# Kernel optimization log

Hardware: AMD Instinct MI355X
Metric: run time of the kernel (lower is better)

Reference implementation:

```python
import jax, jax.numpy as jnp
import numpy as np

DIM = 192
HEADS = 6
WIN = (2, 6, 12)          # (pl, lat, lon)
TOW = 64                  # type_of_windows = (8//2)*(96//6)
N_TOK = WIN[0] * WIN[1] * WIN[2]            # 144
TABLE_ROWS = WIN[0]**2 * WIN[1]**2 * (2 * WIN[2] - 1)  # 3312


def calc_position_bias_indices(size):
    pl, la, lo = size
    plq = np.arange(pl); plk = -np.arange(pl) * pl
    laq = np.arange(la); lak = -np.arange(la) * la
    lon = np.arange(lo)
    gq = np.stack(np.meshgrid(plq, laq, lon, indexing='ij'))  # [3,pl,la,lo]
    gk = np.stack(np.meshgrid(plk, lak, lon, indexing='ij'))
    fq = gq.reshape(3, -1)
    fk = gk.reshape(3, -1)
    d = fq[:, :, None] - fk[:, None, :]          # [3,N,N]
    d = np.transpose(d, (1, 2, 0)).copy()
    d[:, :, 2] += lo - 1
    d[:, :, 1] *= 2 * lo - 1
    d[:, :, 0] *= (2 * lo - 1) * la * la
    return d.sum(-1)                              # [N,N]


def setup_inputs() -> dict:
    key = jax.random.key(0)
    ks = jax.random.split(key, 7)
    B_, nW, N, C = 15, TOW, N_TOK, DIM
    x = jax.random.normal(ks[0], (B_, nW, N, C), jnp.float32)
    mask = jax.random.normal(ks[1], (15, nW, N, N), jnp.float32)  # nLon=15
    qkv_w = jax.random.normal(ks[2], (3 * C, C), jnp.float32) * 0.02
    qkv_b = jnp.zeros((3 * C,), jnp.float32)
    table = jax.random.normal(ks[3], (TABLE_ROWS, TOW, HEADS), jnp.float32) * 0.02
    proj_w = jax.random.normal(ks[4], (C, C), jnp.float32) * 0.02
    proj_b = jnp.zeros((C,), jnp.float32)
    pos_index = jnp.asarray(calc_position_bias_indices(WIN), jnp.int32)  # [N,N]
    return {"x": x, "mask": mask, "qkv_w": qkv_w, "qkv_b": qkv_b,
            "table": table, "proj_w": proj_w, "proj_b": proj_b,
            "pos_index": pos_index}


def reference(x, mask, qkv_w, qkv_b, table, proj_w, proj_b, pos_index):
    B_, nW, N, C = x.shape
    h = HEADS
    hd = C // h
    scale = hd ** -0.5
    # qkv projection -> (3, B_, h, nW, N, hd)
    qkv = (jnp.einsum('bwnc,dc->bwnd', x, qkv_w) + qkv_b)
    qkv = qkv.reshape(B_, nW, N, 3, h, hd).transpose(3, 0, 4, 1, 2, 5)
    q, k, v = qkv[0] * scale, qkv[1], qkv[2]
    attn = jnp.einsum('bhwqd,bhwkd->bhwqk', q, k)      # [B_,h,nW,N,N]
    # gather earth position bias: [N,N,tow,h] -> [h,tow,N,N]
    bias = table[pos_index.reshape(-1)].reshape(N, N, nW, h)
    bias = bias.transpose(3, 2, 0, 1)
    attn = attn + bias[None]
    nLon = mask.shape[0]
    attn = attn.reshape(B_ // nLon, nLon, h, nW, N, N) + mask[None, :, None]
    attn = attn.reshape(B_, h, nW, N, N)
    attn = jax.nn.softmax(attn, axis=-1)
    out = jnp.einsum('bhwqk,bhwkd->bhwqd', attn, v)
    out = out.transpose(0, 2, 3, 1, 4).reshape(B_, nW, N, C)
    return jnp.einsum('bwnc,dc->bwnd', out, proj_w) + proj_b
```

## Files before the change

kernel.cpp:

```cpp
#include <hip/hip_runtime.h>

#define HEADS 6
#define N_TOK 144
#define DIM   192
#define NW    64
#define NB    15
#define NBW   (NB * NW)
#define CHUNK 480

typedef __attribute__((ext_vector_type(8))) short bf16x8;
typedef __attribute__((ext_vector_type(4))) float f32x4;

#define MFMA(a, b, c) __builtin_amdgcn_mfma_f32_16x16x32_bf16(a, b, c, 0, 0, 0)

static __device__ __forceinline__ short f2bf(float f) {
    union { float f; unsigned u; } v; v.f = f;
    unsigned r = v.u + 0x7FFFu + ((v.u >> 16) & 1u);
    return (short)(r >> 16);
}
static __device__ __forceinline__ float bf2f(short s) {
    union { unsigned u; float f; } v;
    v.u = ((unsigned)(unsigned short)s) << 16;
    return v.f;
}

__global__ __launch_bounds__(256)
void bias_k(const float* __restrict__ table, const int* __restrict__ pos_index,
            short* __restrict__ bias_bf) {
    const int t = blockIdx.x;
    for (int e = threadIdx.x; e < N_TOK * N_TOK; e += 256) {
        int idx = pos_index[e];
        bias_bf[(long)t * (N_TOK * N_TOK) + e] = f2bf(table[(long)idx * 384 + t]);
    }
}

__global__ __launch_bounds__(256)
void cvt_k(const float* __restrict__ w, short* __restrict__ o, int n) {
    int i = blockIdx.x * 256 + threadIdx.x;
    if (i < n) o[i] = f2bf(w[i]);
}

__global__ __launch_bounds__(256)
void cvtx_k(const float* __restrict__ x, short* __restrict__ xb, int n4) {
    int i = blockIdx.x * 256 + threadIdx.x;
    if (i < n4) {
        float4 f = ((const float4*)x)[i];
        short4 s = { f2bf(f.x), f2bf(f.y), f2bf(f.z), f2bf(f.w) };
        ((short4*)xb)[i] = s;
    }
}

__global__ __launch_bounds__(576)
void qkvs_k(const short* __restrict__ xb, const short* __restrict__ qkvw_bf,
            const float* __restrict__ qkv_b, short* __restrict__ qkv_out) {
    __shared__ short wlds[192 * 200];

    const int sel = blockIdx.x % 3;
    const int bwL = blockIdx.x / 3;
    const int tid = threadIdx.x;

    for (int u = tid * 8; u < 192 * 192; u += 576 * 8) {
        int r = u / 192, c = u - r * 192;
        *(bf16x8*)&wlds[r * 200 + c] = *(const bf16x8*)&qkvw_bf[sel * 36864 + u];
    }
    __syncthreads();

    const int wid = tid >> 6, lane = tid & 63, lq = lane & 15, lg = lane >> 4;
    const int mg = wid / 3, ng = wid % 3;
    const short* xrow = xb + (long)bwL * N_TOK * DIM;

    f32x4 acc[3][4] = {};
    for (int ks = 0; ks < 6; ++ks) {
        const int k0 = ks * 32 + 8 * lg;
        bf16x8 av[3], bv[4];
        #pragma unroll
        for (int mt = 0; mt < 3; ++mt)
            av[mt] = *(const bf16x8*)&xrow[(mg * 48 + mt * 16 + lq) * DIM + k0];
        #pragma unroll
        for (int nt = 0; nt < 4; ++nt)
            bv[nt] = *(const bf16x8*)&wlds[(ng * 64 + nt * 16 + lq) * 200 + k0];
        #pragma unroll
        for (int mt = 0; mt < 3; ++mt)
            #pragma unroll
            for (int nt = 0; nt < 4; ++nt)
                acc[mt][nt] = MFMA(av[mt], bv[nt], acc[mt][nt]);
    }
    __syncthreads();

    const float scale = 0.17677669529663687f;
    #pragma unroll
    for (int nt = 0; nt < 4; ++nt) {
        const int cd = ng * 64 + nt * 16 + lq;
        const float bb = qkv_b[sel * 192 + cd];
        #pragma unroll
        for (int mt = 0; mt < 3; ++mt)
            #pragma unroll
            for (int i = 0; i < 4; ++i) {
                int row = mg * 48 + mt * 16 + 4 * lg + i;
                float v = acc[mt][nt][i] + bb;
                if (sel == 0) v *= scale;
                wlds[row * 200 + cd] = f2bf(v);
            }
    }
    __syncthreads();

    short* ob = qkv_out + (long)bwL * 6 * 3 * 4608 + (long)sel * 4608;
    #pragma unroll
    for (int j = 0; j < 6; ++j) {
        int u = (j * 576 + tid) * 8;
        int h = u / 4608, rem = u - h * 4608;
        int row = rem >> 5, e = rem & 31;
        *(bf16x8*)&ob[(long)h * 3 * 4608 + rem] =
            *(const bf16x8*)&wlds[row * 200 + h * 32 + e];
    }
}

__global__ __launch_bounds__(576)
void attnproj_k(const short* __restrict__ qkv, const short* __restrict__ bias_bf,
                const float* __restrict__ mask, const short* __restrict__ pwt,
                const float* __restrict__ proj_b, float* __restrict__ out,
                int bw0) {
    __shared__ short pw_s[9 * 16 * 152];
    __shared__ short vlds[32 * 152];
    __shared__ short outb[N_TOK * 200];

    const int bwL = blockIdx.x;
    const int bwG = bw0 + bwL;
    const int tid = threadIdx.x;
    const int lane = tid & 63, lq = lane & 15, lg = lane >> 4;
    const int wid = tid >> 6;
    const int m0 = wid * 16;
    const int w = bwG & 63;
    const float* mp = mask + (long)bwG * (N_TOK * N_TOK);
    short* pw = pw_s + wid * 16 * 152;

    #pragma unroll 1
    for (int h = 0; h < HEADS; ++h) {
        const short* qb = qkv + ((long)(bwL * 6 + h) * 3) * 4608;
        const short* kb = qb + 4608;
        const short* vb = qb + 9216;

        __syncthreads();
        {
            int j = tid >> 2, e0 = (tid & 3) * 8;
            bf16x8 vv = *(const bf16x8*)&vb[j * 32 + e0];
            #pragma unroll
            for (int u = 0; u < 8; ++u) vlds[(e0 + u) * 152 + j] = vv[u];
        }
        __syncthreads();

        const f32x4 zf = {};
        bf16x8 aq = *(const bf16x8*)&qb[(m0 + lq) * 32 + 8 * lg];
        f32x4 lgt[9];
        #pragma unroll
        for (int nt = 0; nt < 9; ++nt) {
            bf16x8 bk = *(const bf16x8*)&kb[(nt * 16 + lq) * 32 + 8 * lg];
            lgt[nt] = MFMA(aq, bk, zf);
        }

        const short* bp = bias_bf + (long)(w * 6 + h) * (N_TOK * N_TOK);
        #pragma unroll
        for (int nt = 0; nt < 9; ++nt)
            #pragma unroll
            for (int i = 0; i < 4; ++i) {
                int r = m0 + 4 * lg + i, c = nt * 16 + lq;
                lgt[nt][i] += bf2f(bp[r * N_TOK + c]) + mp[r * N_TOK + c];
            }

        float inv_s[4];
        #pragma unroll
        for (int i = 0; i < 4; ++i) {
            float m = lgt[0][i];
            #pragma unroll
            for (int nt = 1; nt < 9; ++nt) m = fmaxf(m, lgt[nt][i]);
            m = fmaxf(m, __shfl_xor(m, 1));
            m = fmaxf(m, __shfl_xor(m, 2));
            m = fmaxf(m, __shfl_xor(m, 4));
            m = fmaxf(m, __shfl_xor(m, 8));
            float s = 0.f;
            #pragma unroll
            for (int nt = 0; nt < 9; ++nt) {
                float p = __expf(lgt[nt][i] - m);
                lgt[nt][i] = p;
                s += p;
            }
            s += __shfl_xor(s, 1);
            s += __shfl_xor(s, 2);
            s += __shfl_xor(s, 4);
            s += __shfl_xor(s, 8);
            inv_s[i] = 1.f / s;
        }

        #pragma unroll
        for (int nt = 0; nt < 9; ++nt)
            #pragma unroll
            for (int i = 0; i < 4; ++i)
                pw[(4 * lg + i) * 152 + nt * 16 + lq] = f2bf(lgt[nt][i]);

        f32x4 o[2] = {};
        const bf16x8 zb = {};
        #pragma unroll
        for (int ks = 0; ks < 5; ++ks) {
            bf16x8 ap = *(const bf16x8*)&pw[lq * 152 + ks * 32 + 8 * lg];
            #pragma unroll
            for (int nt = 0; nt < 2; ++nt) {
                bf16x8 bv = *(const bf16x8*)&vlds[(nt * 16 + lq) * 152 + ks * 32 + 8 * lg];
                if (ks == 4 && lg >= 2) { ap = zb; bv = zb; }
                o[nt] = MFMA(ap, bv, o[nt]);
            }
        }

        #pragma unroll
        for (int nt = 0; nt < 2; ++nt)
            #pragma unroll
            for (int i = 0; i < 4; ++i) {
                int row = m0 + 4 * lg + i;
                outb[row * 200 + h * 32 + nt * 16 + lq] = f2bf(o[nt][i] * inv_s[i]);
            }
    }
    __syncthreads();

    f32x4 acc[12] = {};
    for (int ks = 0; ks < 6; ++ks) {
        const int k0 = ks * 32 + 8 * lg;
        bf16x8 a = *(const bf16x8*)&outb[(m0 + lq) * 200 + k0];
        #pragma unroll
        for (int nt = 0; nt < 12; ++nt) {
            bf16x8 b = *(const bf16x8*)&pwt[(nt * 16 + lq) * DIM + k0];
            acc[nt] = MFMA(a, b, acc[nt]);
        }
    }
    float* ob = out + (long)bwG * N_TOK * DIM;
    #pragma unroll
    for (int nt = 0; nt < 12; ++nt) {
        float pb = proj_b[nt * 16 + lq];
        #pragma unroll
        for (int i = 0; i < 4; ++i)
            ob[(m0 + 4 * lg + i) * DIM + nt * 16 + lq] = acc[nt][i] + pb;
    }
}

extern "C" void kernel_launch(void* const* d_in, const int* in_sizes, int n_in,
                              void* d_out, int out_size, void* d_ws, size_t ws_size,
                              hipStream_t stream) {
    const float* x        = (const float*)d_in[0];
    const float* mask     = (const float*)d_in[1];
    const float* qkv_w    = (const float*)d_in[2];
    const float* qkv_b    = (const float*)d_in[3];
    const float* table    = (const float*)d_in[4];
    const float* proj_w   = (const float*)d_in[5];
    const float* proj_b   = (const float*)d_in[6];
    const int*   pos_index= (const int*)d_in[7];
    float* out = (float*)d_out;

    short* bias_bf  = (short*)d_ws;
    short* projw_bf = bias_bf + (size_t)384 * N_TOK * N_TOK;
    short* qkvw_bf  = projw_bf + 36864;
    short* xbf_ws   = qkvw_bf + 110592;
    short* qkv_ws   = xbf_ws + (size_t)CHUNK * N_TOK * DIM;

    bias_k<<<384, 256, 0, stream>>>(table, pos_index, bias_bf);
    cvt_k<<<144, 256, 0, stream>>>(proj_w, projw_bf, DIM * DIM);
    cvt_k<<<432, 256, 0, stream>>>(qkv_w, qkvw_bf, 3 * DIM * DIM);

    const int n4 = CHUNK * N_TOK * DIM / 4;
    for (int c = 0; c < 2; ++c) {
        const int bw0 = c * CHUNK;
        cvtx_k<<<(n4 + 255) / 256, 256, 0, stream>>>(
            x + (long)bw0 * N_TOK * DIM, xbf_ws, n4);
        qkvs_k<<<CHUNK * 3, 576, 0, stream>>>(xbf_ws, qkvw_bf, qkv_b, qkv_ws);
        attnproj_k<<<CHUNK, 576, 0, stream>>>(qkv_ws, bias_bf, mask, projw_bf,
                                              proj_b, out, bw0);
    }
}
```

Measured before the change: 533.2 us.

## Transpose attention MFMA layout, hoist mask loads, split projection into separate kernel

The attention kernel now computes K·Q^T, so each lane owns one query row. Softmax reductions then need only two cross-lane shuffles, and bias and mask can be read as vector loads, with the mask held in registers across all heads. Probabilities are staged through a small per-wave LDS tile, one k-tile at a time, which shrinks LDS use. The output projection moves to a separate kernel that reads a bf16 temporary buffer reusing the x workspace. This trades a global round trip and an extra launch for higher occupancy in the attention kernel.

```diff
diff --git a/kernel.cpp b/kernel.cpp
--- a/kernel.cpp
+++ b/kernel.cpp
@@ -23,6 +23,10 @@
     v.u = ((unsigned)(unsigned short)s) << 16;
     return v.f;
 }
+static __device__ __forceinline__ unsigned pk2(float a, float b) {
+    return (unsigned)(unsigned short)f2bf(a) |
+           ((unsigned)(unsigned short)f2bf(b) << 16);
+}
 
 __global__ __launch_bounds__(256)
 void bias_k(const float* __restrict__ table, const int* __restrict__ pos_index,
@@ -116,23 +120,28 @@
 }
 
 __global__ __launch_bounds__(576)
-void attnproj_k(const short* __restrict__ qkv, const short* __restrict__ bias_bf,
-                const float* __restrict__ mask, const short* __restrict__ pwt,
-                const float* __restrict__ proj_b, float* __restrict__ out,
-                int bw0) {
-    __shared__ short pw_s[9 * 16 * 152];
+void attn3_k(const short* __restrict__ qkv, const short* __restrict__ bias_bf,
+             const float* __restrict__ mask, short* __restrict__ tmp, int bw0) {
     __shared__ short vlds[32 * 152];
-    __shared__ short outb[N_TOK * 200];
+    __shared__ short pws[9 * 16 * 40];
 
     const int bwL = blockIdx.x;
     const int bwG = bw0 + bwL;
     const int tid = threadIdx.x;
     const int lane = tid & 63, lq = lane & 15, lg = lane >> 4;
     const int wid = tid >> 6;
-    const int m0 = wid * 16;
+    const int q = wid * 16 + lq;
     const int w = bwG & 63;
-    const float* mp = mask + (long)bwG * (N_TOK * N_TOK);
-    short* pw = pw_s + wid * 16 * 152;
+
+    const float* mp = mask + (long)bwG * (N_TOK * N_TOK) + q * N_TOK + 4 * lg;
+    float4 mreg[9];
+    #pragma unroll
+    for (int nt = 0; nt < 9; ++nt) mreg[nt] = *(const float4*)&mp[nt * 16];
+
+    short* pw = pws + wid * 16 * 40;
+    short* tb = tmp + (long)bwL * N_TOK * DIM + q * DIM;
+    const f32x4 zf = {};
+    const bf16x8 zb = {};
 
     #pragma unroll 1
     for (int h = 0; h < HEADS; ++h) {
@@ -149,81 +158,91 @@
         }
         __syncthreads();
 
-        const f32x4 zf = {};
-        bf16x8 aq = *(const bf16x8*)&qb[(m0 + lq) * 32 + 8 * lg];
+        bf16x8 bq = *(const bf16x8*)&qb[q * 32 + 8 * lg];
         f32x4 lgt[9];
         #pragma unroll
         for (int nt = 0; nt < 9; ++nt) {
-            bf16x8 bk = *(const bf16x8*)&kb[(nt * 16 + lq) * 32 + 8 * lg];
-            lgt[nt] = MFMA(aq, bk, zf);
-        }
-
-        const short* bp = bias_bf + (long)(w * 6 + h) * (N_TOK * N_TOK);
+            bf16x8 ak = *(const bf16x8*)&kb[(nt * 16 + lq) * 32 + 8 * lg];
+            lgt[nt] = MFMA(ak, bq, zf);
+        }
+
+        const short* bp = bias_bf + (long)(w * 6 + h) * (N_TOK * N_TOK)
+                        + q * N_TOK + 4 * lg;
+        #pragma unroll
+        for (int nt = 0; nt < 9; ++nt) {
+            short4 bs = *(const short4*)&bp[nt * 16];
+            lgt[nt][0] += bf2f(bs.x) + mreg[nt].x;
+            lgt[nt][1] += bf2f(bs.y) + mreg[nt].y;
+            lgt[nt][2] += bf2f(bs.z) + mreg[nt].z;
+            lgt[nt][3] += bf2f(bs.w) + mreg[nt].w;
+        }
+
+        float m = lgt[0][0];
         #pragma unroll
         for (int nt = 0; nt < 9; ++nt)
             #pragma unroll
+            for (int i = 0; i < 4; ++i) m = fmaxf(m, lgt[nt][i]);
+        m = fmaxf(m, __shfl_xor(m, 16));
+        m = fmaxf(m, __shfl_xor(m, 32));
+        float s = 0.f;
+        #pragma unroll
+        for (int nt = 0; nt < 9; ++nt)
+            #pragma unroll
             for (int i = 0; i < 4; ++i) {
-                int r = m0 + 4 * lg + i, c = nt * 16 + lq;
-                lgt[nt][i] += bf2f(bp[r * N_TOK + c]) + mp[r * N_TOK + c];
-            }
-
-        float inv_s[4];
-        #pragma unroll
-        for (int i = 0; i < 4; ++i) {
-            float m = lgt[0][i];
-            #pragma unroll
-            for (int nt = 1; nt < 9; ++nt) m = fmaxf(m, lgt[nt][i]);
-            m = fmaxf(m, __shfl_xor(m, 1));
-            m = fmaxf(m, __shfl_xor(m, 2));
-            m = fmaxf(m, __shfl_xor(m, 4));
-            m = fmaxf(m, __shfl_xor(m, 8));
-            float s = 0.f;
-            #pragma unroll
-            for (int nt = 0; nt < 9; ++nt) {
                 float p = __expf(lgt[nt][i] - m);
                 lgt[nt][i] = p;
                 s += p;
             }
-            s += __shfl_xor(s, 1);
-            s += __shfl_xor(s, 2);
-            s += __shfl_xor(s, 4);
-            s += __shfl_xor(s, 8);
-            inv_s[i] = 1.f / s;
-        }
-
-        #pragma unroll
-        for (int nt = 0; nt < 9; ++nt)
-            #pragma unroll
-            for (int i = 0; i < 4; ++i)
-                pw[(4 * lg + i) * 152 + nt * 16 + lq] = f2bf(lgt[nt][i]);
+        s += __shfl_xor(s, 16);
+        s += __shfl_xor(s, 32);
+        const float inv = 1.f / s;
 
         f32x4 o[2] = {};
-        const bf16x8 zb = {};
-        #pragma unroll
-        for (int ks = 0; ks < 5; ++ks) {
-            bf16x8 ap = *(const bf16x8*)&pw[lq * 152 + ks * 32 + 8 * lg];
-            #pragma unroll
-            for (int nt = 0; nt < 2; ++nt) {
-                bf16x8 bv = *(const bf16x8*)&vlds[(nt * 16 + lq) * 152 + ks * 32 + 8 * lg];
-                if (ks == 4 && lg >= 2) { ap = zb; bv = zb; }
-                o[nt] = MFMA(ap, bv, o[nt]);
-            }
-        }
-
-        #pragma unroll
-        for (int nt = 0; nt < 2; ++nt)
-            #pragma unroll
-            for (int i = 0; i < 4; ++i) {
-                int row = m0 + 4 * lg + i;
-                outb[row * 200 + h * 32 + nt * 16 + lq] = f2bf(o[nt][i] * inv_s[i]);
-            }
-    }
-    __syncthreads();
+        #pragma unroll
+        for (int kt = 0; kt < 5; ++kt) {
+            const int nt0 = 2 * kt;
+            *(unsigned*)&pw[lq * 40 + 4 * lg]     = pk2(lgt[nt0][0], lgt[nt0][1]);
+            *(unsigned*)&pw[lq * 40 + 4 * lg + 2] = pk2(lgt[nt0][2], lgt[nt0][3]);
+            if (kt < 4) {
+                const int nt1 = nt0 + 1;
+                *(unsigned*)&pw[lq * 40 + 16 + 4 * lg]     = pk2(lgt[nt1][0], lgt[nt1][1]);
+                *(unsigned*)&pw[lq * 40 + 16 + 4 * lg + 2] = pk2(lgt[nt1][2], lgt[nt1][3]);
+            }
+            bf16x8 bpf = *(const bf16x8*)&pw[lq * 40 + 8 * lg];
+            #pragma unroll
+            for (int et = 0; et < 2; ++et) {
+                bf16x8 av = *(const bf16x8*)&vlds[(et * 16 + lq) * 152 + kt * 32 + 8 * lg];
+                bf16x8 aa = av, bb = bpf;
+                if (kt == 4 && lg >= 2) { aa = zb; bb = zb; }
+                o[et] = MFMA(aa, bb, o[et]);
+            }
+        }
+
+        #pragma unroll
+        for (int et = 0; et < 2; ++et) {
+            short4 sx = { f2bf(o[et][0] * inv), f2bf(o[et][1] * inv),
+                          f2bf(o[et][2] * inv), f2bf(o[et][3] * inv) };
+            *(short4*)&tb[h * 32 + et * 16 + 4 * lg] = sx;
+        }
+    }
+}
+
+__global__ __launch_bounds__(192)
+void proj_k(const short* __restrict__ tmp, const short* __restrict__ pwt,
+            const float* __restrict__ proj_b, float* __restrict__ out, int bw0) {
+    const int bid = blockIdx.x;
+    const int mthird = bid % 3;
+    const int bwL = bid / 3;
+    const int bwG = bw0 + bwL;
+    const int tid = threadIdx.x;
+    const int wid = tid >> 6, lane = tid & 63, lq = lane & 15, lg = lane >> 4;
+    const int m0 = (mthird * 3 + wid) * 16;
+    const short* tb = tmp + (long)bwL * N_TOK * DIM;
 
     f32x4 acc[12] = {};
     for (int ks = 0; ks < 6; ++ks) {
         const int k0 = ks * 32 + 8 * lg;
-        bf16x8 a = *(const bf16x8*)&outb[(m0 + lq) * 200 + k0];
+        bf16x8 a = *(const bf16x8*)&tb[(m0 + lq) * DIM + k0];
         #pragma unroll
         for (int nt = 0; nt < 12; ++nt) {
             bf16x8 b = *(const bf16x8*)&pwt[(nt * 16 + lq) * DIM + k0];
@@ -257,6 +276,7 @@
     short* projw_bf = bias_bf + (size_t)384 * N_TOK * N_TOK;
     short* qkvw_bf  = projw_bf + 36864;
     short* xbf_ws   = qkvw_bf + 110592;
+    short* tmp_ws   = xbf_ws;
     short* qkv_ws   = xbf_ws + (size_t)CHUNK * N_TOK * DIM;
 
     bias_k<<<384, 256, 0, stream>>>(table, pos_index, bias_bf);
@@ -269,7 +289,7 @@
         cvtx_k<<<(n4 + 255) / 256, 256, 0, stream>>>(
             x + (long)bw0 * N_TOK * DIM, xbf_ws, n4);
         qkvs_k<<<CHUNK * 3, 576, 0, stream>>>(xbf_ws, qkvw_bf, qkv_b, qkv_ws);
-        attnproj_k<<<CHUNK, 576, 0, stream>>>(qkv_ws, bias_bf, mask, projw_bf,
-                                              proj_b, out, bw0);
-    }
-}
+        attn3_k<<<CHUNK, 576, 0, stream>>>(qkv_ws, bias_bf, mask, tmp_ws, bw0);
+        proj_k<<<CHUNK * 3, 192, 0, stream>>>(tmp_ws, projw_bf, proj_b, out, bw0);
+    }
+}
```

Result: faster. 440.0 us (-17.5%).
